# Performance work log

Measured on AMD Instinct MI355X. Metric: run time of the kernel, lower is better.

The kernel has to match this reference:

```python
import jax, jax.numpy as jnp
import numpy as np

B, S, D, N, H, K = 32, 512, 2048, 16, 128, 64
EPS = 1e-6


def setup_inputs() -> dict:
    key = jax.random.key(0)
    ks = jax.random.split(key, 8)
    # glorot-uniform-like scale for the (D, N, H) attention kernels
    kern_scale = (6.0 / (D + H)) ** 0.5
    down_sd = 1.0 / K  # matches module: mean 0, sd = 1/downsampling_k
    q = jax.random.normal(ks[0], (B, S, D), dtype=jnp.float32)
    k = jax.random.normal(ks[1], (B, S, D), dtype=jnp.float32)
    v = jax.random.normal(ks[2], (B, S, D), dtype=jnp.float32)
    query_kernel = jax.random.uniform(ks[3], (D, N, H), jnp.float32, -kern_scale, kern_scale)
    key_kernel = jax.random.uniform(ks[4], (D, N, H), jnp.float32, -kern_scale, kern_scale)
    value_kernel = jax.random.uniform(ks[5], (D, N, H), jnp.float32, -kern_scale, kern_scale)
    key_down = down_sd * jax.random.normal(ks[6], (K, S), dtype=jnp.float32)
    value_down = down_sd * jax.random.normal(ks[7], (K, S), dtype=jnp.float32)
    return dict(q=q, k=k, v=v, query_kernel=query_kernel, key_kernel=key_kernel,
                value_kernel=value_kernel, key_down=key_down, value_down=value_down)


def reference(q, k, v, query_kernel, key_kernel, value_kernel, key_down, value_down):
    # Linformer-style downsampling of keys/values along the sequence axis: [B,S,D] -> [B,K,D]
    key_ds = jnp.einsum('ks,bsd->bkd', key_down, k)
    val_ds = jnp.einsum('ks,bsd->bkd', value_down, v)
    # Per-head projections
    queries = jnp.einsum('bqd,dnh->bqnh', q, query_kernel)   # [B,S,N,H]
    keys = jnp.einsum('bkd,dnh->bknh', key_ds, key_kernel)   # [B,K,N,H]
    values = jnp.einsum('bkd,dnh->bknh', val_ds, value_kernel)  # [B,K,N,H]
    # Kernelized linear attention with elu+1 feature map (mask=False branch)
    phi_q = jax.nn.elu(queries) + 1.0
    phi_k = jax.nn.elu(keys) + 1.0
    s = jnp.einsum('bknd,bknh->bndh', phi_k, values)  # [B,N,H,H]
    z = jnp.sum(phi_k, axis=1)                        # [B,N,H]
    qs = jnp.einsum('bqnd,bndh->bqnh', phi_q, s)      # [B,S,N,H]
    qz = jnp.einsum('bqnd,bnd->bqn', phi_q, z) + EPS  # [B,S,N]
    a_v = qs / qz[..., None]
    return a_v.reshape(B, S, N * H)
```

## Files before the change

### kernel.cpp

```cpp
#include <hip/hip_runtime.h>
#include <cstdint>
#include <cstddef>

typedef float f32x4 __attribute__((ext_vector_type(4)));
typedef short s16x8 __attribute__((ext_vector_type(8)));
typedef unsigned short u16;

#define EPS 1e-6f

__device__ __forceinline__ u16 f2bf(float f) {
    unsigned u = __float_as_uint(f);
    u += 0x7FFFu + ((u >> 16) & 1u);
    return (u16)(u >> 16);
}
__device__ __forceinline__ float bf2f(u16 u) {
    return __uint_as_float(((unsigned)u) << 16);
}

typedef const __attribute__((address_space(1))) void cg_void;
typedef __attribute__((address_space(3))) void l_void;
__device__ __forceinline__ void async16(void* dst_lds, const void* src_g) {
    __builtin_amdgcn_global_load_lds((cg_void*)src_g, (l_void*)dst_lds, 16, 0, 0);
}

#define BARRIER() do { asm volatile("" ::: "memory"); \
                       __builtin_amdgcn_s_barrier();  \
                       asm volatile("" ::: "memory"); } while (0)

__global__ __launch_bounds__(256) void prep_cast(
    const float* __restrict__ q, u16* __restrict__ qb,
    const float* __restrict__ w0, const float* __restrict__ w1,
    const float* __restrict__ w2, u16* __restrict__ o0,
    u16* __restrict__ o1, u16* __restrict__ o2)
{
    __shared__ u16 tl[64 * 68];
    const int bid = blockIdx.x;
    const int tid = threadIdx.x;
    if (bid < 3072) {
        int which = bid >> 10;
        int t = bid & 1023;
        const float* in = which == 0 ? w0 : which == 1 ? w1 : w2;
        u16* out        = which == 0 ? o0 : which == 1 ? o1 : o2;
        int bx = (t & 31) * 64, by = (t >> 5) * 64;
        int tx = tid & 63, ty = tid >> 6;
        #pragma unroll 4
        for (int i = ty; i < 64; i += 4)
            tl[tx * 68 + i] = f2bf(in[(size_t)(by + i) * 2048 + bx + tx]);
        __syncthreads();
        int srow = tid >> 2, sq = tid & 3;
        const u16* lp = &tl[srow * 68 + sq * 16];
        u16* op = &out[(size_t)(bx + srow) * 2048 + by + sq * 16];
        #pragma unroll
        for (int j8 = 0; j8 < 4; ++j8)
            *(short4*)(op + j8 * 4) = *(const short4*)(lp + j8 * 4);
    } else {
        int cb = bid - 3072;
        size_t base = (size_t)cb * 256 + tid;
        #pragma unroll
        for (int it = 0; it < 8; ++it) {
            size_t i = base + (size_t)it * 1048576;
            float4 f = ((const float4*)q)[i];
            ushort4 o;
            o.x = f2bf(f.x); o.y = f2bf(f.y); o.z = f2bf(f.z); o.w = f2bf(f.w);
            ((ushort4*)qb)[i] = o;
        }
    }
}

__global__ __launch_bounds__(256) void down_mfma(
    const float* __restrict__ kin, const float* __restrict__ vin,
    const float* __restrict__ wdk, const float* __restrict__ wdv,
    u16* __restrict__ kds, u16* __restrict__ vds)
{
    __shared__ __align__(16) u16 At[64 * 32];
    __shared__ __align__(16) u16 Bt[128 * 40];
    const int bid = blockIdx.x;
    const int tid = threadIdx.x;
    const int sel = bid >> 9, rem = bid & 511;
    const int b = rem >> 4, d0 = (rem & 15) << 7;
    const float* x  = sel ? vin : kin;
    const float* wd = sel ? wdv : wdk;
    u16* outp       = sel ? vds : kds;
    const int w = tid >> 6, l = tid & 63, l16 = l & 15, k8 = l >> 4;
    f32x4 acc[4][2] = {};
    for (int s0 = 0; s0 < 512; s0 += 32) {
        __syncthreads();
        for (int c = tid; c < 512; c += 256) {
            int kkr = c >> 3, sc = (c & 7) << 2;
            float4 f = *(const float4*)&wd[kkr * 512 + s0 + sc];
            u16* dst = &At[kkr * 32 + sc];
            dst[0] = f2bf(f.x); dst[1] = f2bf(f.y); dst[2] = f2bf(f.z); dst[3] = f2bf(f.w);
        }
        for (int c = tid; c < 512; c += 256) {
            int sp = c >> 5, dq = (c & 31) << 2;
            int srow = sp << 1;
            const float* xp = &x[((size_t)(b * 512) + s0 + srow) * 2048 + d0 + dq];
            float4 f0 = *(const float4*)xp;
            float4 f1 = *(const float4*)(xp + 2048);
            int col = srow ^ ((c & 3) << 3);
            unsigned p0 = (unsigned)f2bf(f0.x) | ((unsigned)f2bf(f1.x) << 16);
            unsigned p1 = (unsigned)f2bf(f0.y) | ((unsigned)f2bf(f1.y) << 16);
            unsigned p2 = (unsigned)f2bf(f0.z) | ((unsigned)f2bf(f1.z) << 16);
            unsigned p3 = (unsigned)f2bf(f0.w) | ((unsigned)f2bf(f1.w) << 16);
            *(unsigned*)&Bt[(dq + 0) * 40 + col] = p0;
            *(unsigned*)&Bt[(dq + 1) * 40 + col] = p1;
            *(unsigned*)&Bt[(dq + 2) * 40 + col] = p2;
            *(unsigned*)&Bt[(dq + 3) * 40 + col] = p3;
        }
        __syncthreads();
        s16x8 af[4], bfr[2];
        #pragma unroll
        for (int fm = 0; fm < 4; ++fm)
            af[fm] = *(const s16x8*)&At[(fm * 16 + l16) * 32 + k8 * 8];
        #pragma unroll
        for (int fn = 0; fn < 2; ++fn)
            bfr[fn] = *(const s16x8*)&Bt[(w * 32 + fn * 16 + l16) * 40
                                         + ((k8 ^ (l16 >> 2)) << 3)];
        #pragma unroll
        for (int fm = 0; fm < 4; ++fm)
            #pragma unroll
            for (int fn = 0; fn < 2; ++fn)
                acc[fm][fn] = __builtin_amdgcn_mfma_f32_16x16x32_bf16(af[fm], bfr[fn], acc[fm][fn], 0, 0, 0);
    }
    #pragma unroll
    for (int fm = 0; fm < 4; ++fm)
        #pragma unroll
        for (int fn = 0; fn < 2; ++fn)
            #pragma unroll
            for (int j = 0; j < 4; ++j) {
                int r = fm * 16 + k8 * 4 + j;
                int c = w * 32 + fn * 16 + l16;
                outp[((size_t)(b * 64 + r)) * 2048 + d0 + c] = f2bf(acc[fm][fn][j]);
            }
}

__global__ __launch_bounds__(512, 2) void gemm256_elu(
    const u16* __restrict__ A, const u16* __restrict__ BT,
    u16* __restrict__ C, int M, int N, int K)
{
    __shared__ __align__(16) u16 lds[8][8192];
    const int tid = threadIdx.x;
    const int w = tid >> 6, l = tid & 63;
    const int wm = w >> 2, wn = w & 3;
    const int l16 = l & 15, k8 = l >> 4;
    const int NT = K >> 6;

    const int nbn = N >> 8;
    const int nwg = gridDim.x;
    int wg = blockIdx.x;
    if ((nwg & 7) == 0) wg = (wg & 7) * (nwg >> 3) + (wg >> 3);
    const int row0 = (wg / nbn) << 8, col0 = (wg % nbn) << 8;

    const int lr  = l >> 3;
    const int scb = (((l & 7) ^ lr) << 4);
    const int swzr = (l16 & 7) << 4;

#define PANEL(s, m, h) (&lds[((s) << 2) | ((m) << 1) | (h)][0])

#define STG(pan, G, prow0, kk0) do {                                             \
        _Pragma("unroll")                                                        \
        for (int i_ = 0; i_ < 2; ++i_) {                                         \
            int seg_ = w + (i_ << 3);                                            \
            const u16* src_ = (G) + (size_t)((prow0) + (seg_ << 3) + lr) * K     \
                              + (kk0) + (scb >> 1);                              \
            async16((pan) + (seg_ << 9), src_);                                  \
        } } while (0)

#define LDA(slot, mh) do { const u16* p_ = PANEL(slot, 0, mh);                   \
        _Pragma("unroll")                                                        \
        for (int fm_ = 0; fm_ < 4; ++fm_)                                        \
        _Pragma("unroll")                                                        \
        for (int ks_ = 0; ks_ < 2; ++ks_)                                        \
            Af[fm_][ks_] = *(const s16x8*)(p_ + (wm * 64 + fm_ * 16 + l16) * 64  \
                           + (((ks_ * 64 + k8 * 16) ^ swzr) >> 1)); } while (0)

#define LDB(slot, nh, dst) do { const u16* p_ = PANEL(slot, 1, nh);              \
        _Pragma("unroll")                                                        \
        for (int fn_ = 0; fn_ < 2; ++fn_)                                        \
        _Pragma("unroll")                                                        \
        for (int ks_ = 0; ks_ < 2; ++ks_)                                        \
            dst[fn_][ks_] = *(const s16x8*)(p_ + (wn * 32 + fn_ * 16 + l16) * 64 \
                           + (((ks_ * 64 + k8 * 16) ^ swzr) >> 1)); } while (0)

#define MM(mh, nh, BF) do {                                                      \
        __builtin_amdgcn_s_setprio(1);                                           \
        _Pragma("unroll")                                                        \
        for (int fm_ = 0; fm_ < 4; ++fm_)                                        \
        _Pragma("unroll")                                                        \
        for (int fn_ = 0; fn_ < 2; ++fn_)                                        \
        _Pragma("unroll")                                                        \
        for (int ks_ = 0; ks_ < 2; ++ks_)                                        \
            acc[mh][nh][fm_][fn_] = __builtin_amdgcn_mfma_f32_16x16x32_bf16(     \
                Af[fm_][ks_], BF[fn_][ks_], acc[mh][nh][fm_][fn_], 0, 0, 0);     \
        __builtin_amdgcn_s_setprio(0); } while (0)

#define TILE(t, cur, nxt, BFc, BFn) do {                                         \
        LDA(cur, 0);                                                             \
        if ((t) + 1 < NT) STG(PANEL(nxt, 0, 1), A, row0 + 128, ((t) + 1) << 6);  \
        BARRIER(); MM(0, 0, BFc); BARRIER();                                     \
        LDB(cur, 1, Bf1);                                                        \
        if ((t) + 2 < NT) STG(PANEL(cur, 0, 0), A, row0, ((t) + 2) << 6);        \
        BARRIER(); MM(0, 1, Bf1); BARRIER();                                     \
        LDA(cur, 1);                                                             \
        if ((t) + 2 < NT) STG(PANEL(cur, 1, 0), BT, col0, ((t) + 2) << 6);       \
        BARRIER(); MM(1, 1, Bf1); BARRIER();                                     \
        if ((t) + 2 < NT) STG(PANEL(cur, 1, 1), BT, col0 + 128, ((t) + 2) << 6); \
        BARRIER(); MM(1, 0, BFc);                                                \
        if ((t) == NT - 2)     asm volatile("s_waitcnt vmcnt(0)" ::: "memory");  \
        else if ((t) < NT - 2) asm volatile("s_waitcnt vmcnt(6)" ::: "memory");  \
        BARRIER();                                                               \
        if ((t) + 1 < NT) LDB(nxt, 0, BFn);                                      \
    } while (0)

    f32x4 acc[2][2][4][2] = {};
    s16x8 Af[4][2], Bf0a[2][2], Bf0b[2][2], Bf1[2][2];

    STG(PANEL(0, 0, 0), A,  row0,       0);
    STG(PANEL(0, 1, 0), BT, col0,       0);
    STG(PANEL(0, 1, 1), BT, col0 + 128, 0);
    STG(PANEL(0, 0, 1), A,  row0 + 128, 0);
    STG(PANEL(1, 0, 0), A,  row0,       64);
    STG(PANEL(1, 1, 0), BT, col0,       64);
    STG(PANEL(1, 1, 1), BT, col0 + 128, 64);
    asm volatile("s_waitcnt vmcnt(6)" ::: "memory");
    BARRIER();
    LDB(0, 0, Bf0a);

    for (int t = 0; t < NT; t += 2) {
        TILE(t,     0, 1, Bf0a, Bf0b);
        TILE(t + 1, 1, 0, Bf0b, Bf0a);
    }
#undef PANEL
#undef STG
#undef LDA
#undef LDB
#undef MM
#undef TILE

    #pragma unroll
    for (int mh = 0; mh < 2; ++mh)
        #pragma unroll
        for (int fm = 0; fm < 4; ++fm)
            #pragma unroll
            for (int j = 0; j < 4; ++j) {
                int r = row0 + mh * 128 + wm * 64 + fm * 16 + k8 * 4 + j;
                size_t rb = (size_t)r * N;
                #pragma unroll
                for (int nh = 0; nh < 2; ++nh)
                    #pragma unroll
                    for (int fn = 0; fn < 2; ++fn) {
                        int c = col0 + nh * 128 + wn * 32 + fn * 16 + l16;
                        float x = acc[mh][nh][fm][fn][j];
                        x = x > 0.0f ? x + 1.0f : __expf(x);
                        C[rb + c] = f2bf(x);
                    }
            }
}

__global__ __launch_bounds__(256) void gemm128_dual(
    const u16* __restrict__ A0, const u16* __restrict__ B0, u16* __restrict__ C0,
    const u16* __restrict__ A1, const u16* __restrict__ B1, u16* __restrict__ C1)
{
    const u16* A  = blockIdx.z ? A1 : A0;
    const u16* BT = blockIdx.z ? B1 : B0;
    u16* C        = blockIdx.z ? C1 : C0;
    const bool elu = (blockIdx.z == 0);
    const int K = 2048;

    __shared__ __align__(16) u16 lds[2][8192];
    const int tid = threadIdx.x;
    const int w = tid >> 6, l = tid & 63;
    const int wm = w >> 1, wn = w & 1;
    const int l16 = l & 15, k8 = l >> 4;
    const int sr = (w << 4) + (l >> 2);
    const int sc = (l & 3) << 3;
    const int row0 = blockIdx.y * 128, col0 = blockIdx.x * 128;
    const int nk = K >> 5;
    f32x4 acc[4][4] = {};

#define STAGE(buf, kt) do {                                                        \
        int kk0 = (kt) << 5;                                                       \
        _Pragma("unroll")                                                          \
        for (int i = 0; i < 2; ++i) {                                              \
            const u16* ga = A + (size_t)(row0 + i * 64 + sr) * K + kk0 + sc;       \
            async16(&lds[buf][i * 2048 + (w << 9)], ga);                           \
            const u16* gb = BT + (size_t)(col0 + i * 64 + sr) * K + kk0 + sc;      \
            async16(&lds[buf][4096 + i * 2048 + (w << 9)], gb);                    \
        }                                                                          \
    } while (0)

    STAGE(0, 0);
    asm volatile("s_waitcnt vmcnt(0)" ::: "memory");
    __syncthreads();
    int cur = 0;
    for (int kt = 0; kt < nk; ++kt) {
        if (kt + 1 < nk) STAGE(cur ^ 1, kt + 1);
        s16x8 af[4], bfr[4];
        const u16* Ab = &lds[cur][0];
        const u16* Bb = &lds[cur][4096];
        #pragma unroll
        for (int fm = 0; fm < 4; ++fm)
            af[fm] = *(const s16x8*)&Ab[((wm << 6) + (fm << 4) + l16) * 32 + (k8 << 3)];
        #pragma unroll
        for (int fn = 0; fn < 4; ++fn)
            bfr[fn] = *(const s16x8*)&Bb[((wn << 6) + (fn << 4) + l16) * 32 + (k8 << 3)];
        #pragma unroll
        for (int fm = 0; fm < 4; ++fm)
            #pragma unroll
            for (int fn = 0; fn < 4; ++fn)
                acc[fm][fn] = __builtin_amdgcn_mfma_f32_16x16x32_bf16(af[fm], bfr[fn], acc[fm][fn], 0, 0, 0);
        __syncthreads();
        cur ^= 1;
    }
#undef STAGE

    #pragma unroll
    for (int fm = 0; fm < 4; ++fm)
        #pragma unroll
        for (int j = 0; j < 4; ++j) {
            int r = row0 + (wm << 6) + (fm << 4) + (k8 << 2) + j;
            size_t rbase = (size_t)r * 2048;
            #pragma unroll
            for (int fn = 0; fn < 4; ++fn) {
                int c = col0 + (wn << 6) + (fn << 4) + l16;
                float x = acc[fm][fn][j];
                if (elu) x = x > 0.0f ? x + 1.0f : __expf(x);
                C[rbase + c] = f2bf(x);
            }
        }
}

__global__ __launch_bounds__(256) void qs_fused(
    const u16* __restrict__ phiq, const u16* __restrict__ phik,
    const u16* __restrict__ vals, float* __restrict__ out)
{
    __shared__ __align__(16) u16 pk[64 * 128];
    __shared__ __align__(16) u16 vv[64 * 128];
    __shared__ __align__(16) u16 Blds[128 * 128];
    __shared__ float zl[128];
    const int bn = blockIdx.x;
    const int b = bn >> 4, n = bn & 15;
    const int tid = threadIdx.x;
    const int w = tid >> 6, l = tid & 63;
    const int l16 = l & 15, k8 = l >> 4;

    for (int i = tid; i < 1024; i += 256) {
        size_t g = ((size_t)(b * 64 + (i >> 4))) * 2048 + n * 128 + ((i & 15) << 3);
        async16(&pk[i << 3], &phik[g]);
        async16(&vv[i << 3], &vals[g]);
    }
    asm volatile("s_waitcnt vmcnt(0)" ::: "memory");
    __syncthreads();

    {
        int hg = tid >> 4, dg = tid & 15;
        int h0 = hg * 8, d0 = dg * 8;
        float acc[8][8] = {};
        for (int kk = 0; kk < 64; ++kk) {
            s16x8 vr = *(const s16x8*)&vv[kk * 128 + h0];
            s16x8 pr = *(const s16x8*)&pk[kk * 128 + d0];
            float va[8], pa[8];
            #pragma unroll
            for (int i = 0; i < 8; ++i) { va[i] = bf2f((u16)vr[i]); pa[i] = bf2f((u16)pr[i]); }
            #pragma unroll
            for (int i = 0; i < 8; ++i)
                #pragma unroll
                for (int j = 0; j < 8; ++j)
                    acc[i][j] += va[i] * pa[j];
        }
        if (tid < 128) {
            float s = 0.0f;
            for (int kk = 0; kk < 64; ++kk) s += bf2f(pk[kk * 128 + tid]);
            zl[tid] = s;
        }
        #pragma unroll
        for (int i = 0; i < 8; ++i) {
            int row = h0 + i;
            u16 rowv[8];
            #pragma unroll
            for (int j = 0; j < 8; ++j) rowv[j] = f2bf(acc[i][j]);
            int boff = (dg << 4) ^ ((row & 7) << 4);
            *(s16x8*)&Blds[row * 128 + (boff >> 1)] = *(s16x8*)rowv;
        }
    }
    __syncthreads();

    const int swz = (l16 & 7) << 4;
    s16x8 Bz[4];
    #pragma unroll
    for (int ks = 0; ks < 4; ++ks) {
        const float* zp = &zl[(ks << 5) + (k8 << 3)];
        float4 f0 = *(const float4*)zp;
        float4 f1 = *(const float4*)(zp + 4);
        u16 tmp[8] = { f2bf(f0.x), f2bf(f0.y), f2bf(f0.z), f2bf(f0.w),
                       f2bf(f1.x), f2bf(f1.y), f2bf(f1.z), f2bf(f1.w) };
        Bz[ks] = *(const s16x8*)tmp;
    }

    for (int rb = 0; rb < 4; ++rb) {
        const size_t arow0 = (size_t)(b * 512 + rb * 128);
        s16x8 Af[2][4];
        #pragma unroll
        for (int fm = 0; fm < 2; ++fm)
            #pragma unroll
            for (int ks = 0; ks < 4; ++ks) {
                int row = (w << 5) + (fm << 4) + l16;
                Af[fm][ks] = *(const s16x8*)(phiq + (arow0 + row) * 2048 + n * 128
                                             + (ks << 5) + (k8 << 3));
            }
        f32x4 accz[2] = {};
        #pragma unroll
        for (int fm = 0; fm < 2; ++fm)
            #pragma unroll
            for (int ks = 0; ks < 4; ++ks)
                accz[fm] = __builtin_amdgcn_mfma_f32_16x16x32_bf16(Af[fm][ks], Bz[ks], accz[fm], 0, 0, 0);

        f32x4 acc2[2][8] = {};
        #pragma unroll
        for (int fn = 0; fn < 8; ++fn) {
            s16x8 Bfr[4];
            #pragma unroll
            for (int ks = 0; ks < 4; ++ks)
                Bfr[ks] = *(const s16x8*)&Blds[((fn << 4) + l16) * 128
                                               + ((((ks << 6) + (k8 << 4)) ^ swz) >> 1)];
            #pragma unroll
            for (int fm = 0; fm < 2; ++fm)
                #pragma unroll
                for (int ks = 0; ks < 4; ++ks)
                    acc2[fm][fn] = __builtin_amdgcn_mfma_f32_16x16x32_bf16(Af[fm][ks], Bfr[ks], acc2[fm][fn], 0, 0, 0);
        }

        #pragma unroll
        for (int fm = 0; fm < 2; ++fm)
            #pragma unroll
            for (int j = 0; j < 4; ++j) {
                int row = (w << 5) + (fm << 4) + (k8 << 2) + j;
                float rq = 1.0f / (accz[fm][j] + EPS);
                size_t ob = (arow0 + row) * 2048 + n * 128;
                #pragma unroll
                for (int fn = 0; fn < 8; ++fn)
                    out[ob + (fn << 4) + l16] = acc2[fm][fn][j] * rq;
            }
    }
}

extern "C" void kernel_launch(void* const* d_in, const int* in_sizes, int n_in,
                              void* d_out, int out_size, void* d_ws, size_t ws_size,
                              hipStream_t stream) {
    (void)in_sizes; (void)n_in; (void)out_size; (void)ws_size;
    const float* q   = (const float*)d_in[0];
    const float* k   = (const float*)d_in[1];
    const float* v   = (const float*)d_in[2];
    const float* wq  = (const float*)d_in[3];
    const float* wk  = (const float*)d_in[4];
    const float* wv  = (const float*)d_in[5];
    const float* kdw = (const float*)d_in[6];
    const float* vdw = (const float*)d_in[7];
    float* out = (float*)d_out;

    char* p = (char*)d_ws;
    u16* qb   = (u16*)p; p += (size_t)16384 * 2048 * 2;
    u16* wqT  = (u16*)p; p += (size_t)2048 * 2048 * 2;
    u16* wkT  = (u16*)p; p += (size_t)2048 * 2048 * 2;
    u16* wvT  = (u16*)p; p += (size_t)2048 * 2048 * 2;
    u16* kds  = (u16*)p; p += (size_t)2048 * 2048 * 2;
    u16* vds  = (u16*)p; p += (size_t)2048 * 2048 * 2;
    u16* phiq = (u16*)p; p += (size_t)16384 * 2048 * 2;
    u16* phik = (u16*)p; p += (size_t)2048 * 2048 * 2;
    u16* vals = (u16*)p; p += (size_t)2048 * 2048 * 2;

    prep_cast<<<7168, 256, 0, stream>>>(q, qb, wq, wk, wv, wqT, wkT, wvT);
    down_mfma<<<1024, 256, 0, stream>>>(k, v, kdw, vdw, kds, vds);
    gemm128_dual<<<dim3(16, 16, 2), 256, 0, stream>>>(kds, wkT, phik, vds, wvT, vals);
    gemm256_elu<<<512, 512, 0, stream>>>(qb, wqT, phiq, 16384, 2048, 2048);
    qs_fused<<<512, 256, 0, stream>>>(phiq, phik, vals, out);
}
```

Measured before the change: 374.1 us.

## Merge K/V projection GEMMs into Q GEMM launch and halve down-projection tile width

The separate 128x128 dual GEMM for the key/value projections is removed, and its work is folded into the 256x256 query-projection GEMM kernel as extra row blocks (640 workgroups total), with a per-block select of operands and of the ELU epilogue. The Linformer down-sampling kernel now uses 64-column tiles instead of 128, doubling its grid to 2048 blocks with one B fragment per wave. This removes one kernel launch and the tail of the small GEMM, and lets the K/V work fill the large GEMM's grid. The down kernel gains parallelism but each block does less MFMA work per staged A tile.

```diff
diff --git a/kernel.cpp b/kernel.cpp
--- a/kernel.cpp
+++ b/kernel.cpp
@@ -73,16 +73,18 @@
     u16* __restrict__ kds, u16* __restrict__ vds)
 {
     __shared__ __align__(16) u16 At[64 * 32];
-    __shared__ __align__(16) u16 Bt[128 * 40];
+    __shared__ __align__(16) u16 Bt[64 * 40];
     const int bid = blockIdx.x;
     const int tid = threadIdx.x;
-    const int sel = bid >> 9, rem = bid & 511;
-    const int b = rem >> 4, d0 = (rem & 15) << 7;
+    const int sel = bid >> 10, rem = bid & 1023;
+    const int b = rem >> 5, d0 = (rem & 31) << 6;
     const float* x  = sel ? vin : kin;
     const float* wd = sel ? wdv : wdk;
     u16* outp       = sel ? vds : kds;
     const int w = tid >> 6, l = tid & 63, l16 = l & 15, k8 = l >> 4;
-    f32x4 acc[4][2] = {};
+    f32x4 acc[4];
+    #pragma unroll
+    for (int fm = 0; fm < 4; ++fm) acc[fm] = (f32x4){0.f, 0.f, 0.f, 0.f};
     for (int s0 = 0; s0 < 512; s0 += 32) {
         __syncthreads();
         for (int c = tid; c < 512; c += 256) {
@@ -91,8 +93,9 @@
             u16* dst = &At[kkr * 32 + sc];
             dst[0] = f2bf(f.x); dst[1] = f2bf(f.y); dst[2] = f2bf(f.z); dst[3] = f2bf(f.w);
         }
-        for (int c = tid; c < 512; c += 256) {
-            int sp = c >> 5, dq = (c & 31) << 2;
+        {
+            int c = tid;
+            int sp = c >> 4, dq = (c & 15) << 2;
             int srow = sp << 1;
             const float* xp = &x[((size_t)(b * 512) + s0 + srow) * 2048 + d0 + dq];
             float4 f0 = *(const float4*)xp;
@@ -108,48 +111,47 @@
             *(unsigned*)&Bt[(dq + 3) * 40 + col] = p3;
         }
         __syncthreads();
-        s16x8 af[4], bfr[2];
+        s16x8 af[4], bfr;
         #pragma unroll
         for (int fm = 0; fm < 4; ++fm)
             af[fm] = *(const s16x8*)&At[(fm * 16 + l16) * 32 + k8 * 8];
-        #pragma unroll
-        for (int fn = 0; fn < 2; ++fn)
-            bfr[fn] = *(const s16x8*)&Bt[(w * 32 + fn * 16 + l16) * 40
-                                         + ((k8 ^ (l16 >> 2)) << 3)];
+        bfr = *(const s16x8*)&Bt[((w << 4) + l16) * 40 + ((k8 ^ (l16 >> 2)) << 3)];
         #pragma unroll
         for (int fm = 0; fm < 4; ++fm)
-            #pragma unroll
-            for (int fn = 0; fn < 2; ++fn)
-                acc[fm][fn] = __builtin_amdgcn_mfma_f32_16x16x32_bf16(af[fm], bfr[fn], acc[fm][fn], 0, 0, 0);
+            acc[fm] = __builtin_amdgcn_mfma_f32_16x16x32_bf16(af[fm], bfr, acc[fm], 0, 0, 0);
     }
     #pragma unroll
     for (int fm = 0; fm < 4; ++fm)
         #pragma unroll
-        for (int fn = 0; fn < 2; ++fn)
-            #pragma unroll
-            for (int j = 0; j < 4; ++j) {
-                int r = fm * 16 + k8 * 4 + j;
-                int c = w * 32 + fn * 16 + l16;
-                outp[((size_t)(b * 64 + r)) * 2048 + d0 + c] = f2bf(acc[fm][fn][j]);
-            }
-}
-
-__global__ __launch_bounds__(512, 2) void gemm256_elu(
-    const u16* __restrict__ A, const u16* __restrict__ BT,
-    u16* __restrict__ C, int M, int N, int K)
+        for (int j = 0; j < 4; ++j) {
+            int r = fm * 16 + k8 * 4 + j;
+            int c = (w << 4) + l16;
+            outp[((size_t)(b * 64 + r)) * 2048 + d0 + c] = f2bf(acc[fm][j]);
+        }
+}
+
+__global__ __launch_bounds__(512, 2) void gemm256_tri(
+    const u16* __restrict__ qb,  const u16* __restrict__ kds, const u16* __restrict__ vds,
+    const u16* __restrict__ wqT, const u16* __restrict__ wkT, const u16* __restrict__ wvT,
+    u16* __restrict__ phiq, u16* __restrict__ phik, u16* __restrict__ vals)
 {
+    const int K = 2048, N = 2048;
+    const int NT = 32;
+    const int nbn = 8;
     __shared__ __align__(16) u16 lds[8][8192];
     const int tid = threadIdx.x;
     const int w = tid >> 6, l = tid & 63;
     const int wm = w >> 2, wn = w & 3;
     const int l16 = l & 15, k8 = l >> 4;
-    const int NT = K >> 6;
-
-    const int nbn = N >> 8;
-    const int nwg = gridDim.x;
+
     int wg = blockIdx.x;
-    if ((nwg & 7) == 0) wg = (wg & 7) * (nwg >> 3) + (wg >> 3);
-    const int row0 = (wg / nbn) << 8, col0 = (wg % nbn) << 8;
+    wg = (wg & 7) * 80 + (wg >> 3);
+    const int rbx = wg / nbn;
+    const int col0 = (wg % nbn) << 8;
+    const u16* A; const u16* BT; u16* C; bool eluF; int row0;
+    if (rbx < 64)      { A = qb;  BT = wqT; C = phiq; eluF = true;  row0 = rbx << 8; }
+    else if (rbx < 72) { A = kds; BT = wkT; C = phik; eluF = true;  row0 = (rbx - 64) << 8; }
+    else               { A = vds; BT = wvT; C = vals; eluF = false; row0 = (rbx - 72) << 8; }
 
     const int lr  = l >> 3;
     const int scb = (((l & 7) ^ lr) << 4);
@@ -251,83 +253,10 @@
                     for (int fn = 0; fn < 2; ++fn) {
                         int c = col0 + nh * 128 + wn * 32 + fn * 16 + l16;
                         float x = acc[mh][nh][fm][fn][j];
-                        x = x > 0.0f ? x + 1.0f : __expf(x);
+                        if (eluF) x = x > 0.0f ? x + 1.0f : __expf(x);
                         C[rb + c] = f2bf(x);
                     }
             }
-}
-
-__global__ __launch_bounds__(256) void gemm128_dual(
-    const u16* __restrict__ A0, const u16* __restrict__ B0, u16* __restrict__ C0,
-    const u16* __restrict__ A1, const u16* __restrict__ B1, u16* __restrict__ C1)
-{
-    const u16* A  = blockIdx.z ? A1 : A0;
-    const u16* BT = blockIdx.z ? B1 : B0;
-    u16* C        = blockIdx.z ? C1 : C0;
-    const bool elu = (blockIdx.z == 0);
-    const int K = 2048;
-
-    __shared__ __align__(16) u16 lds[2][8192];
-    const int tid = threadIdx.x;
-    const int w = tid >> 6, l = tid & 63;
-    const int wm = w >> 1, wn = w & 1;
-    const int l16 = l & 15, k8 = l >> 4;
-    const int sr = (w << 4) + (l >> 2);
-    const int sc = (l & 3) << 3;
-    const int row0 = blockIdx.y * 128, col0 = blockIdx.x * 128;
-    const int nk = K >> 5;
-    f32x4 acc[4][4] = {};
-
-#define STAGE(buf, kt) do {                                                        \
-        int kk0 = (kt) << 5;                                                       \
-        _Pragma("unroll")                                                          \
-        for (int i = 0; i < 2; ++i) {                                              \
-            const u16* ga = A + (size_t)(row0 + i * 64 + sr) * K + kk0 + sc;       \
-            async16(&lds[buf][i * 2048 + (w << 9)], ga);                           \
-            const u16* gb = BT + (size_t)(col0 + i * 64 + sr) * K + kk0 + sc;      \
-            async16(&lds[buf][4096 + i * 2048 + (w << 9)], gb);                    \
-        }                                                                          \
-    } while (0)
-
-    STAGE(0, 0);
-    asm volatile("s_waitcnt vmcnt(0)" ::: "memory");
-    __syncthreads();
-    int cur = 0;
-    for (int kt = 0; kt < nk; ++kt) {
-        if (kt + 1 < nk) STAGE(cur ^ 1, kt + 1);
-        s16x8 af[4], bfr[4];
-        const u16* Ab = &lds[cur][0];
-        const u16* Bb = &lds[cur][4096];
-        #pragma unroll
-        for (int fm = 0; fm < 4; ++fm)
-            af[fm] = *(const s16x8*)&Ab[((wm << 6) + (fm << 4) + l16) * 32 + (k8 << 3)];
-        #pragma unroll
-        for (int fn = 0; fn < 4; ++fn)
-            bfr[fn] = *(const s16x8*)&Bb[((wn << 6) + (fn << 4) + l16) * 32 + (k8 << 3)];
-        #pragma unroll
-        for (int fm = 0; fm < 4; ++fm)
-            #pragma unroll
-            for (int fn = 0; fn < 4; ++fn)
-                acc[fm][fn] = __builtin_amdgcn_mfma_f32_16x16x32_bf16(af[fm], bfr[fn], acc[fm][fn], 0, 0, 0);
-        __syncthreads();
-        cur ^= 1;
-    }
-#undef STAGE
-
-    #pragma unroll
-    for (int fm = 0; fm < 4; ++fm)
-        #pragma unroll
-        for (int j = 0; j < 4; ++j) {
-            int r = row0 + (wm << 6) + (fm << 4) + (k8 << 2) + j;
-            size_t rbase = (size_t)r * 2048;
-            #pragma unroll
-            for (int fn = 0; fn < 4; ++fn) {
-                int c = col0 + (wn << 6) + (fn << 4) + l16;
-                float x = acc[fm][fn][j];
-                if (elu) x = x > 0.0f ? x + 1.0f : __expf(x);
-                C[rbase + c] = f2bf(x);
-            }
-        }
 }
 
 __global__ __launch_bounds__(256) void qs_fused(
@@ -470,8 +399,7 @@
     u16* vals = (u16*)p; p += (size_t)2048 * 2048 * 2;
 
     prep_cast<<<7168, 256, 0, stream>>>(q, qb, wq, wk, wv, wqT, wkT, wvT);
-    down_mfma<<<1024, 256, 0, stream>>>(k, v, kdw, vdw, kds, vds);
-    gemm128_dual<<<dim3(16, 16, 2), 256, 0, stream>>>(kds, wkT, phik, vds, wvT, vals);
-    gemm256_elu<<<512, 512, 0, stream>>>(qb, wqT, phiq, 16384, 2048, 2048);
+    down_mfma<<<2048, 256, 0, stream>>>(k, v, kdw, vdw, kds, vds);
+    gemm256_tri<<<640, 512, 0, stream>>>(qb, kds, vds, wqT, wkT, wvT, phiq, phik, vals);
     qs_fused<<<512, 256, 0, stream>>>(phiq, phik, vals, out);
 }
```

Result: no change. 377.1 us (+0.8%).

## Fuse phi_q GEMM epilogue with qs/qz attention, split S/Z kernel, narrow downsample tiles

Applied to the files above, without the earlier changes.

The large Q projection GEMM now applies elu+1 in its epilogue, stages the phi_q tile in LDS with a swizzle, and immediately multiplies it by the per-head S matrix and z vector to write the final output. The 64 MiB bf16 phi_q intermediate is no longer written to and read back from global memory. S and z are computed once per (batch, head) in a separate sz_kernel and read from global by the fused GEMM. The downsampling kernel also switches to 64-column tiles with twice as many blocks. The trade-offs are a longer epilogue, which may reduce overlap, and S fragments fetched from global or L2 instead of LDS.

```diff
diff --git a/kernel.cpp b/kernel.cpp
--- a/kernel.cpp
+++ b/kernel.cpp
@@ -73,16 +73,18 @@
     u16* __restrict__ kds, u16* __restrict__ vds)
 {
     __shared__ __align__(16) u16 At[64 * 32];
-    __shared__ __align__(16) u16 Bt[128 * 40];
+    __shared__ __align__(16) u16 Bt[64 * 40];
     const int bid = blockIdx.x;
     const int tid = threadIdx.x;
-    const int sel = bid >> 9, rem = bid & 511;
-    const int b = rem >> 4, d0 = (rem & 15) << 7;
+    const int sel = bid >> 10, rem = bid & 1023;
+    const int b = rem >> 5, d0 = (rem & 31) << 6;
     const float* x  = sel ? vin : kin;
     const float* wd = sel ? wdv : wdk;
     u16* outp       = sel ? vds : kds;
     const int w = tid >> 6, l = tid & 63, l16 = l & 15, k8 = l >> 4;
-    f32x4 acc[4][2] = {};
+    f32x4 acc[4];
+    #pragma unroll
+    for (int fm = 0; fm < 4; ++fm) acc[fm] = (f32x4){0.f, 0.f, 0.f, 0.f};
     for (int s0 = 0; s0 < 512; s0 += 32) {
         __syncthreads();
         for (int c = tid; c < 512; c += 256) {
@@ -91,8 +93,9 @@
             u16* dst = &At[kkr * 32 + sc];
             dst[0] = f2bf(f.x); dst[1] = f2bf(f.y); dst[2] = f2bf(f.z); dst[3] = f2bf(f.w);
         }
-        for (int c = tid; c < 512; c += 256) {
-            int sp = c >> 5, dq = (c & 31) << 2;
+        {
+            int c = tid;
+            int sp = c >> 4, dq = (c & 15) << 2;
             int srow = sp << 1;
             const float* xp = &x[((size_t)(b * 512) + s0 + srow) * 2048 + d0 + dq];
             float4 f0 = *(const float4*)xp;
@@ -108,44 +111,155 @@
             *(unsigned*)&Bt[(dq + 3) * 40 + col] = p3;
         }
         __syncthreads();
-        s16x8 af[4], bfr[2];
+        s16x8 af[4], bfr;
         #pragma unroll
         for (int fm = 0; fm < 4; ++fm)
             af[fm] = *(const s16x8*)&At[(fm * 16 + l16) * 32 + k8 * 8];
-        #pragma unroll
-        for (int fn = 0; fn < 2; ++fn)
-            bfr[fn] = *(const s16x8*)&Bt[(w * 32 + fn * 16 + l16) * 40
-                                         + ((k8 ^ (l16 >> 2)) << 3)];
+        bfr = *(const s16x8*)&Bt[((w << 4) + l16) * 40 + ((k8 ^ (l16 >> 2)) << 3)];
         #pragma unroll
         for (int fm = 0; fm < 4; ++fm)
-            #pragma unroll
-            for (int fn = 0; fn < 2; ++fn)
-                acc[fm][fn] = __builtin_amdgcn_mfma_f32_16x16x32_bf16(af[fm], bfr[fn], acc[fm][fn], 0, 0, 0);
+            acc[fm] = __builtin_amdgcn_mfma_f32_16x16x32_bf16(af[fm], bfr, acc[fm], 0, 0, 0);
     }
     #pragma unroll
     for (int fm = 0; fm < 4; ++fm)
         #pragma unroll
-        for (int fn = 0; fn < 2; ++fn)
-            #pragma unroll
-            for (int j = 0; j < 4; ++j) {
-                int r = fm * 16 + k8 * 4 + j;
-                int c = w * 32 + fn * 16 + l16;
-                outp[((size_t)(b * 64 + r)) * 2048 + d0 + c] = f2bf(acc[fm][fn][j]);
+        for (int j = 0; j < 4; ++j) {
+            int r = fm * 16 + k8 * 4 + j;
+            int c = (w << 4) + l16;
+            outp[((size_t)(b * 64 + r)) * 2048 + d0 + c] = f2bf(acc[fm][j]);
+        }
+}
+
+__global__ __launch_bounds__(256) void gemm128_dual(
+    const u16* __restrict__ A0, const u16* __restrict__ B0, u16* __restrict__ C0,
+    const u16* __restrict__ A1, const u16* __restrict__ B1, u16* __restrict__ C1)
+{
+    const u16* A  = blockIdx.z ? A1 : A0;
+    const u16* BT = blockIdx.z ? B1 : B0;
+    u16* C        = blockIdx.z ? C1 : C0;
+    const bool elu = (blockIdx.z == 0);
+    const int K = 2048;
+
+    __shared__ __align__(16) u16 lds[2][8192];
+    const int tid = threadIdx.x;
+    const int w = tid >> 6, l = tid & 63;
+    const int wm = w >> 1, wn = w & 1;
+    const int l16 = l & 15, k8 = l >> 4;
+    const int sr = (w << 4) + (l >> 2);
+    const int sc = (l & 3) << 3;
+    const int row0 = blockIdx.y * 128, col0 = blockIdx.x * 128;
+    const int nk = K >> 5;
+    f32x4 acc[4][4] = {};
+
+#define STAGE(buf, kt) do {                                                        \
+        int kk0 = (kt) << 5;                                                       \
+        _Pragma("unroll")                                                          \
+        for (int i = 0; i < 2; ++i) {                                              \
+            const u16* ga = A + (size_t)(row0 + i * 64 + sr) * K + kk0 + sc;       \
+            async16(&lds[buf][i * 2048 + (w << 9)], ga);                           \
+            const u16* gb = BT + (size_t)(col0 + i * 64 + sr) * K + kk0 + sc;      \
+            async16(&lds[buf][4096 + i * 2048 + (w << 9)], gb);                    \
+        }                                                                          \
+    } while (0)
+
+    STAGE(0, 0);
+    asm volatile("s_waitcnt vmcnt(0)" ::: "memory");
+    __syncthreads();
+    int cur = 0;
+    for (int kt = 0; kt < nk; ++kt) {
+        if (kt + 1 < nk) STAGE(cur ^ 1, kt + 1);
+        s16x8 af[4], bfr[4];
+        const u16* Ab = &lds[cur][0];
+        const u16* Bb = &lds[cur][4096];
+        #pragma unroll
+        for (int fm = 0; fm < 4; ++fm)
+            af[fm] = *(const s16x8*)&Ab[((wm << 6) + (fm << 4) + l16) * 32 + (k8 << 3)];
+        #pragma unroll
+        for (int fn = 0; fn < 4; ++fn)
+            bfr[fn] = *(const s16x8*)&Bb[((wn << 6) + (fn << 4) + l16) * 32 + (k8 << 3)];
+        #pragma unroll
+        for (int fm = 0; fm < 4; ++fm)
+            #pragma unroll
+            for (int fn = 0; fn < 4; ++fn)
+                acc[fm][fn] = __builtin_amdgcn_mfma_f32_16x16x32_bf16(af[fm], bfr[fn], acc[fm][fn], 0, 0, 0);
+        __syncthreads();
+        cur ^= 1;
+    }
+#undef STAGE
+
+    #pragma unroll
+    for (int fm = 0; fm < 4; ++fm)
+        #pragma unroll
+        for (int j = 0; j < 4; ++j) {
+            int r = row0 + (wm << 6) + (fm << 4) + (k8 << 2) + j;
+            size_t rbase = (size_t)r * 2048;
+            #pragma unroll
+            for (int fn = 0; fn < 4; ++fn) {
+                int c = col0 + (wn << 6) + (fn << 4) + l16;
+                float x = acc[fm][fn][j];
+                if (elu) x = x > 0.0f ? x + 1.0f : __expf(x);
+                C[rbase + c] = f2bf(x);
             }
-}
-
-__global__ __launch_bounds__(512, 2) void gemm256_elu(
+        }
+}
+
+__global__ __launch_bounds__(256) void sz_kernel(
+    const u16* __restrict__ phik, const u16* __restrict__ vals,
+    u16* __restrict__ sT, float* __restrict__ z)
+{
+    int b = blockIdx.x >> 4, n = blockIdx.x & 15;
+    __shared__ __align__(16) u16 pk[64 * 128];
+    __shared__ __align__(16) u16 vv[64 * 128];
+    int tid = threadIdx.x;
+    for (int i = tid; i < 1024; i += 256) {
+        int r = i >> 4, c8 = (i & 15) << 3;
+        size_t g = ((size_t)(b * 64 + r)) * 2048 + n * 128 + c8;
+        ((s16x8*)pk)[i] = *(const s16x8*)&phik[g];
+        ((s16x8*)vv)[i] = *(const s16x8*)&vals[g];
+    }
+    __syncthreads();
+    if (tid < 128) {
+        float s = 0.0f;
+        for (int kk = 0; kk < 64; ++kk) s += bf2f(pk[kk * 128 + tid]);
+        z[((size_t)(b * 16 + n)) * 128 + tid] = s;
+    }
+    int hg = tid >> 4, dg = tid & 15;
+    int h0 = hg * 8, d0 = dg * 8;
+    float acc[8][8] = {};
+    for (int kk = 0; kk < 64; ++kk) {
+        s16x8 vr = *(const s16x8*)&vv[kk * 128 + h0];
+        s16x8 pr = *(const s16x8*)&pk[kk * 128 + d0];
+        float va[8], pa[8];
+        #pragma unroll
+        for (int i = 0; i < 8; ++i) { va[i] = bf2f((u16)vr[i]); pa[i] = bf2f((u16)pr[i]); }
+        #pragma unroll
+        for (int i = 0; i < 8; ++i)
+            #pragma unroll
+            for (int j = 0; j < 8; ++j)
+                acc[i][j] += va[i] * pa[j];
+    }
+    size_t base = ((size_t)(b * 16 + n)) * 16384;
+    #pragma unroll
+    for (int i = 0; i < 8; ++i) {
+        u16 row[8];
+        #pragma unroll
+        for (int j = 0; j < 8; ++j) row[j] = f2bf(acc[i][j]);
+        *(s16x8*)&sT[base + (size_t)(h0 + i) * 128 + d0] = *(s16x8*)row;
+    }
+}
+
+__global__ __launch_bounds__(512, 2) void gemm256_qs(
     const u16* __restrict__ A, const u16* __restrict__ BT,
-    u16* __restrict__ C, int M, int N, int K)
+    const u16* __restrict__ sT, const float* __restrict__ z,
+    float* __restrict__ outp)
 {
+    const int K = 2048, N = 2048, NT = 32, nbn = 8;
     __shared__ __align__(16) u16 lds[8][8192];
     const int tid = threadIdx.x;
     const int w = tid >> 6, l = tid & 63;
     const int wm = w >> 2, wn = w & 3;
     const int l16 = l & 15, k8 = l >> 4;
-    const int NT = K >> 6;
-
-    const int nbn = N >> 8;
+
     const int nwg = gridDim.x;
     int wg = blockIdx.x;
     if ((nwg & 7) == 0) wg = (wg & 7) * (nwg >> 3) + (wg >> 3);
@@ -237,183 +351,66 @@
 #undef MM
 #undef TILE
 
+    const int b = row0 >> 9;
+    const int n0 = col0 >> 7;
+    u16* P = &lds[0][0];
+
     #pragma unroll
     for (int mh = 0; mh < 2; ++mh)
         #pragma unroll
         for (int fm = 0; fm < 4; ++fm)
             #pragma unroll
             for (int j = 0; j < 4; ++j) {
-                int r = row0 + mh * 128 + wm * 64 + fm * 16 + k8 * 4 + j;
-                size_t rb = (size_t)r * N;
+                int rr = mh * 128 + wm * 64 + fm * 16 + k8 * 4 + j;
+                int rowbase = rr * 256;
+                int msk = ((rr >> 2) & 7) << 4;
                 #pragma unroll
                 for (int nh = 0; nh < 2; ++nh)
                     #pragma unroll
                     for (int fn = 0; fn < 2; ++fn) {
-                        int c = col0 + nh * 128 + wn * 32 + fn * 16 + l16;
+                        int cc = nh * 128 + wn * 32 + fn * 16 + l16;
                         float x = acc[mh][nh][fm][fn][j];
                         x = x > 0.0f ? x + 1.0f : __expf(x);
-                        C[rb + c] = f2bf(x);
+                        P[rowbase + (cc ^ msk)] = f2bf(x);
                     }
             }
-}
-
-__global__ __launch_bounds__(256) void gemm128_dual(
-    const u16* __restrict__ A0, const u16* __restrict__ B0, u16* __restrict__ C0,
-    const u16* __restrict__ A1, const u16* __restrict__ B1, u16* __restrict__ C1)
-{
-    const u16* A  = blockIdx.z ? A1 : A0;
-    const u16* BT = blockIdx.z ? B1 : B0;
-    u16* C        = blockIdx.z ? C1 : C0;
-    const bool elu = (blockIdx.z == 0);
-    const int K = 2048;
-
-    __shared__ __align__(16) u16 lds[2][8192];
-    const int tid = threadIdx.x;
-    const int w = tid >> 6, l = tid & 63;
-    const int wm = w >> 1, wn = w & 1;
-    const int l16 = l & 15, k8 = l >> 4;
-    const int sr = (w << 4) + (l >> 2);
-    const int sc = (l & 3) << 3;
-    const int row0 = blockIdx.y * 128, col0 = blockIdx.x * 128;
-    const int nk = K >> 5;
-    f32x4 acc[4][4] = {};
-
-#define STAGE(buf, kt) do {                                                        \
-        int kk0 = (kt) << 5;                                                       \
-        _Pragma("unroll")                                                          \
-        for (int i = 0; i < 2; ++i) {                                              \
-            const u16* ga = A + (size_t)(row0 + i * 64 + sr) * K + kk0 + sc;       \
-            async16(&lds[buf][i * 2048 + (w << 9)], ga);                           \
-            const u16* gb = BT + (size_t)(col0 + i * 64 + sr) * K + kk0 + sc;      \
-            async16(&lds[buf][4096 + i * 2048 + (w << 9)], gb);                    \
-        }                                                                          \
-    } while (0)
-
-    STAGE(0, 0);
-    asm volatile("s_waitcnt vmcnt(0)" ::: "memory");
     __syncthreads();
-    int cur = 0;
-    for (int kt = 0; kt < nk; ++kt) {
-        if (kt + 1 < nk) STAGE(cur ^ 1, kt + 1);
-        s16x8 af[4], bfr[4];
-        const u16* Ab = &lds[cur][0];
-        const u16* Bb = &lds[cur][4096];
-        #pragma unroll
-        for (int fm = 0; fm < 4; ++fm)
-            af[fm] = *(const s16x8*)&Ab[((wm << 6) + (fm << 4) + l16) * 32 + (k8 << 3)];
-        #pragma unroll
-        for (int fn = 0; fn < 4; ++fn)
-            bfr[fn] = *(const s16x8*)&Bb[((wn << 6) + (fn << 4) + l16) * 32 + (k8 << 3)];
-        #pragma unroll
-        for (int fm = 0; fm < 4; ++fm)
-            #pragma unroll
-            for (int fn = 0; fn < 4; ++fn)
-                acc[fm][fn] = __builtin_amdgcn_mfma_f32_16x16x32_bf16(af[fm], bfr[fn], acc[fm][fn], 0, 0, 0);
-        __syncthreads();
-        cur ^= 1;
-    }
-#undef STAGE
-
-    #pragma unroll
-    for (int fm = 0; fm < 4; ++fm)
-        #pragma unroll
-        for (int j = 0; j < 4; ++j) {
-            int r = row0 + (wm << 6) + (fm << 4) + (k8 << 2) + j;
-            size_t rbase = (size_t)r * 2048;
-            #pragma unroll
-            for (int fn = 0; fn < 4; ++fn) {
-                int c = col0 + (wn << 6) + (fn << 4) + l16;
-                float x = acc[fm][fn][j];
-                if (elu) x = x > 0.0f ? x + 1.0f : __expf(x);
-                C[rbase + c] = f2bf(x);
+
+    for (int nsel = 0; nsel < 2; ++nsel) {
+        const int nn = n0 + nsel;
+        const size_t stb = ((size_t)(b * 16 + nn)) << 14;
+        const float* zp0 = z + ((size_t)(b * 16 + nn) << 7);
+
+        s16x8 Bz[4];
+        #pragma unroll
+        for (int ks = 0; ks < 4; ++ks) {
+            const float* zp = zp0 + (ks << 5) + (k8 << 3);
+            float4 f0 = *(const float4*)zp;
+            float4 f1 = *(const float4*)(zp + 4);
+            u16 tmp[8] = { f2bf(f0.x), f2bf(f0.y), f2bf(f0.z), f2bf(f0.w),
+                           f2bf(f1.x), f2bf(f1.y), f2bf(f1.z), f2bf(f1.w) };
+            Bz[ks] = *(const s16x8*)tmp;
+        }
+
+        s16x8 Af2[2][4];
+        #pragma unroll
+        for (int fm2 = 0; fm2 < 2; ++fm2) {
+            int rr = (w << 5) + (fm2 << 4) + l16;
+            int rowbase = rr * 256;
+            int msk = ((rr >> 2) & 7) << 4;
+            #pragma unroll
+            for (int ks = 0; ks < 4; ++ks) {
+                int cc = (nsel << 7) + (ks << 5) + (k8 << 3);
+                Af2[fm2][ks] = *(const s16x8*)&P[rowbase + (cc ^ msk)];
             }
         }
-}
-
-__global__ __launch_bounds__(256) void qs_fused(
-    const u16* __restrict__ phiq, const u16* __restrict__ phik,
-    const u16* __restrict__ vals, float* __restrict__ out)
-{
-    __shared__ __align__(16) u16 pk[64 * 128];
-    __shared__ __align__(16) u16 vv[64 * 128];
-    __shared__ __align__(16) u16 Blds[128 * 128];
-    __shared__ float zl[128];
-    const int bn = blockIdx.x;
-    const int b = bn >> 4, n = bn & 15;
-    const int tid = threadIdx.x;
-    const int w = tid >> 6, l = tid & 63;
-    const int l16 = l & 15, k8 = l >> 4;
-
-    for (int i = tid; i < 1024; i += 256) {
-        size_t g = ((size_t)(b * 64 + (i >> 4))) * 2048 + n * 128 + ((i & 15) << 3);
-        async16(&pk[i << 3], &phik[g]);
-        async16(&vv[i << 3], &vals[g]);
-    }
-    asm volatile("s_waitcnt vmcnt(0)" ::: "memory");
-    __syncthreads();
-
-    {
-        int hg = tid >> 4, dg = tid & 15;
-        int h0 = hg * 8, d0 = dg * 8;
-        float acc[8][8] = {};
-        for (int kk = 0; kk < 64; ++kk) {
-            s16x8 vr = *(const s16x8*)&vv[kk * 128 + h0];
-            s16x8 pr = *(const s16x8*)&pk[kk * 128 + d0];
-            float va[8], pa[8];
-            #pragma unroll
-            for (int i = 0; i < 8; ++i) { va[i] = bf2f((u16)vr[i]); pa[i] = bf2f((u16)pr[i]); }
-            #pragma unroll
-            for (int i = 0; i < 8; ++i)
-                #pragma unroll
-                for (int j = 0; j < 8; ++j)
-                    acc[i][j] += va[i] * pa[j];
-        }
-        if (tid < 128) {
-            float s = 0.0f;
-            for (int kk = 0; kk < 64; ++kk) s += bf2f(pk[kk * 128 + tid]);
-            zl[tid] = s;
-        }
-        #pragma unroll
-        for (int i = 0; i < 8; ++i) {
-            int row = h0 + i;
-            u16 rowv[8];
-            #pragma unroll
-            for (int j = 0; j < 8; ++j) rowv[j] = f2bf(acc[i][j]);
-            int boff = (dg << 4) ^ ((row & 7) << 4);
-            *(s16x8*)&Blds[row * 128 + (boff >> 1)] = *(s16x8*)rowv;
-        }
-    }
-    __syncthreads();
-
-    const int swz = (l16 & 7) << 4;
-    s16x8 Bz[4];
-    #pragma unroll
-    for (int ks = 0; ks < 4; ++ks) {
-        const float* zp = &zl[(ks << 5) + (k8 << 3)];
-        float4 f0 = *(const float4*)zp;
-        float4 f1 = *(const float4*)(zp + 4);
-        u16 tmp[8] = { f2bf(f0.x), f2bf(f0.y), f2bf(f0.z), f2bf(f0.w),
-                       f2bf(f1.x), f2bf(f1.y), f2bf(f1.z), f2bf(f1.w) };
-        Bz[ks] = *(const s16x8*)tmp;
-    }
-
-    for (int rb = 0; rb < 4; ++rb) {
-        const size_t arow0 = (size_t)(b * 512 + rb * 128);
-        s16x8 Af[2][4];
-        #pragma unroll
-        for (int fm = 0; fm < 2; ++fm)
-            #pragma unroll
-            for (int ks = 0; ks < 4; ++ks) {
-                int row = (w << 5) + (fm << 4) + l16;
-                Af[fm][ks] = *(const s16x8*)(phiq + (arow0 + row) * 2048 + n * 128
-                                             + (ks << 5) + (k8 << 3));
-            }
+
         f32x4 accz[2] = {};
         #pragma unroll
-        for (int fm = 0; fm < 2; ++fm)
+        for (int fm2 = 0; fm2 < 2; ++fm2)
             #pragma unroll
             for (int ks = 0; ks < 4; ++ks)
-                accz[fm] = __builtin_amdgcn_mfma_f32_16x16x32_bf16(Af[fm][ks], Bz[ks], accz[fm], 0, 0, 0);
+                accz[fm2] = __builtin_amdgcn_mfma_f32_16x16x32_bf16(Af2[fm2][ks], Bz[ks], accz[fm2], 0, 0, 0);
 
         f32x4 acc2[2][8] = {};
         #pragma unroll
@@ -421,25 +418,25 @@
             s16x8 Bfr[4];
             #pragma unroll
             for (int ks = 0; ks < 4; ++ks)
-                Bfr[ks] = *(const s16x8*)&Blds[((fn << 4) + l16) * 128
-                                               + ((((ks << 6) + (k8 << 4)) ^ swz) >> 1)];
-            #pragma unroll
-            for (int fm = 0; fm < 2; ++fm)
+                Bfr[ks] = *(const s16x8*)&sT[stb + (size_t)((fn << 4) + l16) * 128
+                                             + (ks << 5) + (k8 << 3)];
+            #pragma unroll
+            for (int fm2 = 0; fm2 < 2; ++fm2)
                 #pragma unroll
                 for (int ks = 0; ks < 4; ++ks)
-                    acc2[fm][fn] = __builtin_amdgcn_mfma_f32_16x16x32_bf16(Af[fm][ks], Bfr[ks], acc2[fm][fn], 0, 0, 0);
-        }
-
-        #pragma unroll
-        for (int fm = 0; fm < 2; ++fm)
+                    acc2[fm2][fn] = __builtin_amdgcn_mfma_f32_16x16x32_bf16(Af2[fm2][ks], Bfr[ks], acc2[fm2][fn], 0, 0, 0);
+        }
+
+        #pragma unroll
+        for (int fm2 = 0; fm2 < 2; ++fm2)
             #pragma unroll
             for (int j = 0; j < 4; ++j) {
-                int row = (w << 5) + (fm << 4) + (k8 << 2) + j;
-                float rq = 1.0f / (accz[fm][j] + EPS);
-                size_t ob = (arow0 + row) * 2048 + n * 128;
+                int grow = row0 + (w << 5) + (fm2 << 4) + (k8 << 2) + j;
+                float rq = 1.0f / (accz[fm2][j] + EPS);
+                size_t ob = (size_t)grow * 2048 + col0 + (nsel << 7);
                 #pragma unroll
                 for (int fn = 0; fn < 8; ++fn)
-                    out[ob + (fn << 4) + l16] = acc2[fm][fn][j] * rq;
+                    outp[ob + (fn << 4) + l16] = acc2[fm2][fn][j] * rq;
             }
     }
 }
@@ -465,13 +462,14 @@
     u16* wvT  = (u16*)p; p += (size_t)2048 * 2048 * 2;
     u16* kds  = (u16*)p; p += (size_t)2048 * 2048 * 2;
     u16* vds  = (u16*)p; p += (size_t)2048 * 2048 * 2;
-    u16* phiq = (u16*)p; p += (size_t)16384 * 2048 * 2;
     u16* phik = (u16*)p; p += (size_t)2048 * 2048 * 2;
     u16* vals = (u16*)p; p += (size_t)2048 * 2048 * 2;
+    u16* sT   = (u16*)p; p += (size_t)512 * 128 * 128 * 2;
+    float* z  = (float*)p; p += (size_t)512 * 128 * 4;
 
     prep_cast<<<7168, 256, 0, stream>>>(q, qb, wq, wk, wv, wqT, wkT, wvT);
-    down_mfma<<<1024, 256, 0, stream>>>(k, v, kdw, vdw, kds, vds);
+    down_mfma<<<2048, 256, 0, stream>>>(k, v, kdw, vdw, kds, vds);
     gemm128_dual<<<dim3(16, 16, 2), 256, 0, stream>>>(kds, wkT, phik, vds, wvT, vals);
-    gemm256_elu<<<512, 512, 0, stream>>>(qb, wqT, phiq, 16384, 2048, 2048);
-    qs_fused<<<512, 256, 0, stream>>>(phiq, phik, vals, out);
-}
+    sz_kernel<<<512, 256, 0, stream>>>(phik, vals, sT, z);
+    gemm256_qs<<<512, 512, 0, stream>>>(qb, wqT, sT, z, out);
+}
```

New measurement: 374.7 us. About the same (+0.2%).
